# Kernel optimization log

Hardware: AMD Instinct MI355X
Metric: run time of the kernel (lower is better)

## Reference

```python
import jax, jax.numpy as jnp
import numpy as np

B, S, D, H = 4, 2048, 768, 4
DH = D // H  # 192


def setup_inputs() -> dict:
    key = jax.random.key(0)
    ks = jax.random.split(key, 5)
    std = 1.0 / np.sqrt(D)
    return {
        "x": jax.random.normal(ks[0], (B, S, D), dtype=jnp.float32),
        "Wq": jax.random.normal(ks[1], (D, D), dtype=jnp.float32) * std,
        "Wk": jax.random.normal(ks[2], (D, D), dtype=jnp.float32) * std,
        "Wv": jax.random.normal(ks[3], (D, D), dtype=jnp.float32) * std,
        "Wo": jax.random.normal(ks[4], (D, D), dtype=jnp.float32) * std,
    }


def reference(x, Wq, Wk, Wv, Wo):
    b, s, d = x.shape
    # nn.Linear(bias=False): y = x @ W.T
    q = (x @ Wq.T).reshape(b, s, H, DH).transpose(0, 2, 1, 3)  # [B,H,S,DH]
    k = (x @ Wk.T).reshape(b, s, H, DH).transpose(0, 2, 1, 3)
    v = (x @ Wv.T).reshape(b, s, H, DH).transpose(0, 2, 1, 3)
    scale = jnp.sqrt(jnp.asarray(DH, dtype=q.dtype))
    logits = jnp.einsum("bhqd,bhkd->bhqk", q, k) / scale  # [B,H,S,S]
    causal = jnp.tril(jnp.ones((s, s), dtype=bool))
    logits = jnp.where(causal, logits, -jnp.inf)
    A = jax.nn.softmax(logits, axis=-1)
    preout = jnp.einsum("bhqk,bhkd->bhqd", A, v)  # [B,H,S,DH]
    # W_O = rearrange(Wo.T, '(h dh) dm -> h dh dm'); sum over heads == full Wo
    W_O = Wo.T.reshape(H, DH, D)
    out = jnp.einsum("bhsd,hdm->bsm", preout, W_O)  # [B,S,D]
    return out
```

## Files before the change

kernel.cpp:

```cpp
#include <hip/hip_runtime.h>
#include <hip/hip_bf16.h>

constexpr int CB = 4, CS = 2048, CD = 768, CH = 4, CDH = 192;
constexpr int CM = CB * CS;

typedef float f32x4 __attribute__((ext_vector_type(4)));
typedef float fx4 __attribute__((ext_vector_type(4)));
typedef __bf16 bx8 __attribute__((ext_vector_type(8)));
typedef unsigned short u16;
typedef u16 u16x8 __attribute__((ext_vector_type(8)));
typedef u16 u16x4 __attribute__((ext_vector_type(4)));

static __device__ __forceinline__ u16 f32_bf16(float f) {
  unsigned u = __builtin_bit_cast(unsigned, f);
  u += 0x7FFFu + ((u >> 16) & 1u);
  return (u16)(u >> 16);
}
static __device__ __forceinline__ float bf16_f32(u16 v) {
  return __builtin_bit_cast(float, (unsigned)v << 16);
}

static __device__ __forceinline__ f32x4 mfma16(bx8 a, bx8 b, f32x4 c) {
  return __builtin_amdgcn_mfma_f32_16x16x32_bf16(a, b, c, 0, 0, 0);
}

static __device__ __forceinline__ void bar_bare() {
  __builtin_amdgcn_s_barrier();
  __builtin_amdgcn_sched_barrier(0);
}
static __device__ __forceinline__ void bar_lgkm() {
  asm volatile("s_waitcnt lgkmcnt(0)" ::: "memory");
  __builtin_amdgcn_s_barrier();
  __builtin_amdgcn_sched_barrier(0);
}

__global__ void __launch_bounds__(256) convert_all(
    const float* __restrict__ x, const float* __restrict__ wq,
    const float* __restrict__ wk, const float* __restrict__ wv,
    const float* __restrict__ wo, u16* __restrict__ xb, u16* __restrict__ wqb,
    u16* __restrict__ wkb, u16* __restrict__ wvb, u16* __restrict__ wob) {
  const float* srcs[5] = {x, wq, wk, wv, wo};
  u16* dsts[5] = {xb, wqb, wkb, wvb, wob};
  const int n4s[5] = {CM * CD / 4, CD * CD / 4, CD * CD / 4, CD * CD / 4,
                      CD * CD / 4};
  const int gsz = gridDim.x * blockDim.x;
  const int gid = blockIdx.x * blockDim.x + threadIdx.x;
#pragma unroll
  for (int sg = 0; sg < 5; ++sg) {
    const fx4* src = (const fx4*)srcs[sg];
    u16* dst = dsts[sg];
    const int n4 = n4s[sg];
    for (int i = gid; i < n4; i += gsz) {
      fx4 v = src[i];
      u16x4 o;
      o[0] = f32_bf16(v[0]);
      o[1] = f32_bf16(v[1]);
      o[2] = f32_bf16(v[2]);
      o[3] = f32_bf16(v[3]);
      *(u16x4*)&dst[(size_t)i * 4] = o;
    }
  }
}

template <bool OUT_BF16>
__global__ void __launch_bounds__(256) gemm_bt(
    const u16* __restrict__ A, const u16* __restrict__ Bw0,
    const u16* __restrict__ Bw1, const u16* __restrict__ Bw2,
    void* __restrict__ C0, void* __restrict__ C1, void* __restrict__ C2,
    int M, int N, int K) {
  constexpr int LDK = 72;
  __shared__ u16 As[128][LDK];
  __shared__ u16 Bs[128][LDK];
  const int z = blockIdx.z;
  const u16* Bw = (z == 0) ? Bw0 : ((z == 1) ? Bw1 : Bw2);
  void* Cv = (z == 0) ? C0 : ((z == 1) ? C1 : C2);
  const int m0 = blockIdx.x * 128;
  const int n0 = blockIdx.y * 128;
  const int tid = threadIdx.x;
  const int wave = tid >> 6, lane = tid & 63;
  const int wr = wave >> 1, wc = wave & 1;
  const int lr = lane & 15, lhi = lane >> 4;

  f32x4 acc[4][4];
  const f32x4 zero = {0.f, 0.f, 0.f, 0.f};
#pragma unroll
  for (int i = 0; i < 4; ++i)
#pragma unroll
    for (int j = 0; j < 4; ++j) acc[i][j] = zero;

  u16x8 areg[4], breg[4];
  auto ldregs = [&](int kk) {
#pragma unroll
    for (int r = 0; r < 4; ++r) {
      const int id = tid + r * 256;
      const int row = id >> 3, ch = id & 7;
      areg[r] = *(const u16x8*)&A[(size_t)(m0 + row) * K + kk + ch * 8];
      breg[r] = *(const u16x8*)&Bw[(size_t)(n0 + row) * K + kk + ch * 8];
    }
  };

  ldregs(0);
  for (int kk = 0; kk < K; kk += 64) {
    bar_bare();
#pragma unroll
    for (int r = 0; r < 4; ++r) {
      const int id = tid + r * 256;
      const int row = id >> 3, ch = id & 7;
      *(u16x8*)&As[row][ch * 8] = areg[r];
      *(u16x8*)&Bs[row][ch * 8] = breg[r];
    }
    if (kk + 64 < K) ldregs(kk + 64);
    bar_lgkm();
#pragma unroll
    for (int ks = 0; ks < 2; ++ks) {
      bx8 af[4], bf[4];
#pragma unroll
      for (int mf = 0; mf < 4; ++mf)
        af[mf] = *(const bx8*)&As[wr * 64 + mf * 16 + lr][ks * 32 + lhi * 8];
#pragma unroll
      for (int nf = 0; nf < 4; ++nf)
        bf[nf] = *(const bx8*)&Bs[wc * 64 + nf * 16 + lr][ks * 32 + lhi * 8];
      __builtin_amdgcn_s_setprio(1);
#pragma unroll
      for (int mf = 0; mf < 4; ++mf)
#pragma unroll
        for (int nf = 0; nf < 4; ++nf)
          acc[mf][nf] = mfma16(af[mf], bf[nf], acc[mf][nf]);
      __builtin_amdgcn_s_setprio(0);
    }
  }
#pragma unroll
  for (int mf = 0; mf < 4; ++mf)
#pragma unroll
    for (int nf = 0; nf < 4; ++nf)
#pragma unroll
      for (int r = 0; r < 4; ++r) {
        const int row = m0 + wr * 64 + mf * 16 + lhi * 4 + r;
        const int col = n0 + wc * 64 + nf * 16 + lr;
        if constexpr (OUT_BF16)
          ((u16*)Cv)[(size_t)row * N + col] = f32_bf16(acc[mf][nf][r]);
        else
          ((float*)Cv)[(size_t)row * N + col] = acc[mf][nf][r];
      }
}

__global__ void __launch_bounds__(256, 2) flash_attn(
    const u16* __restrict__ Qg, const u16* __restrict__ Kg,
    const u16* __restrict__ Vg, u16* __restrict__ Og, u16* __restrict__ paO,
    float* __restrict__ paML, u16* __restrict__ pbO,
    float* __restrict__ pbML) {
  __shared__ u16 Ks[12288];
  __shared__ u16 Vs[12288];
  const int i0_ = blockIdx.x;
  const int xcd = i0_ & 7;
  const int j_ = i0_ >> 3;
  const int bh = xcd * 2 + (j_ >> 5);
  const int jj = j_ & 31;
  const int t = jj >> 1;
  const int roleB = jj & 1;
  const int qtLo = t, qtHi = 31 - t;
  const int slot = bh * 16 + (15 - t);
  const int b = bh >> 2, h = bh & 3;
  const int tid = threadIdx.x;
  const int wave = tid >> 6, lane = tid & 63;
  const int lr = lane & 15, lhi = lane >> 4;
  const size_t base_elem = ((size_t)b * CS) * CD + (size_t)h * CDH;
  constexpr float scale = 0.07216878364870323f;
  const f32x4 zero = {0.f, 0.f, 0.f, 0.f};

  int kOff[6], vOff[6];
#pragma unroll
  for (int r = 0; r < 6; ++r) {
    const int p = tid + r * 256;
    {
      const int k = p / 24, c16 = p - k * 24;
      const unsigned swz = ((unsigned)(c16 * 16)) ^ ((unsigned)((k & 7) << 4));
      kOff[r] = k * CD + (int)(swz >> 1);
    }
    {
      const int blk = p >> 3, kq = (p >> 1) & 3, dh = p & 1;
      const int kpos = ((blk & 15) << 2) + kq;
      const int kglob = (((kpos >> 5) * 2 + ((kpos >> 2) & 1)) << 4) +
                        (((kpos >> 3) & 3) << 2) + (kpos & 3);
      const int d = ((blk >> 4) << 4) + dh * 8;
      vOff[r] = kglob * CD + d;
    }
  }
  const unsigned vlds0 =
      (unsigned)(unsigned long long)(__attribute__((address_space(3)))
                                         u16*)&Vs[0];

  float m_run, l_run;
  f32x4 acc[12];
  bx8 qf[6];
  u16x8 kreg[6], vreg[6];

  auto qload = [&](int qt) {
    const size_t qoff = base_elem + (size_t)(qt * 64 + wave * 16 + lr) * CD;
#pragma unroll
    for (int c = 0; c < 6; ++c)
      qf[c] = *(const bx8*)&Qg[qoff + c * 32 + lhi * 8];
  };

  auto ldregs = [&](int kt) {
    const u16* kg = Kg + base_elem + (size_t)(kt * 64) * CD;
    const u16* vg = Vg + base_elem + (size_t)(kt * 64) * CD;
#pragma unroll
    for (int r = 0; r < 6; ++r) {
      kreg[r] = *(const u16x8*)&kg[kOff[r]];
      vreg[r] = *(const u16x8*)&vg[vOff[r]];
    }
  };

  auto compute = [&](int i, int qt) {
    const int qg = qt * 64 + wave * 16 + lr;
    const int k0 = i * 64;
    const bool diag = (i == qt);
    f32x4 st[4];
#pragma unroll
    for (int mf = 0; mf < 4; ++mf) st[mf] = zero;
    __builtin_amdgcn_s_setprio(1);
#pragma unroll
    for (int c = 0; c < 6; ++c)
#pragma unroll
      for (int mf = 0; mf < 4; ++mf) {
        const int row = mf * 16 + lr;
        const unsigned off =
            ((unsigned)(c * 64 + lhi * 16)) ^ ((unsigned)((row & 7) << 4));
        const bx8 kf =
            *(const bx8*)((const char*)Ks + (size_t)row * 384 + off);
        st[mf] = mfma16(kf, qf[c], st[mf]);
      }
    __builtin_amdgcn_s_setprio(0);
    float pvv[16];
#pragma unroll
    for (int mf = 0; mf < 4; ++mf)
#pragma unroll
      for (int r = 0; r < 4; ++r) {
        float s = st[mf][r] * scale;
        if (diag && (k0 + mf * 16 + lhi * 4 + r > qg)) s = -INFINITY;
        pvv[mf * 4 + r] = s;
      }
    float mx = pvv[0];
#pragma unroll
    for (int tt = 1; tt < 16; ++tt) mx = fmaxf(mx, pvv[tt]);
    mx = fmaxf(mx, __shfl_xor(mx, 16, 64));
    mx = fmaxf(mx, __shfl_xor(mx, 32, 64));
    const bool skip = __all(mx - m_run <= 8.0f);
    if (!skip) {
      const float mnew = fmaxf(m_run, mx);
      const float alpha = __expf(m_run - mnew);
      float afr[4];
#pragma unroll
      for (int r = 0; r < 4; ++r) afr[r] = __shfl(alpha, lhi * 4 + r, 64);
#pragma unroll
      for (int nf = 0; nf < 12; ++nf)
#pragma unroll
        for (int r = 0; r < 4; ++r) acc[nf][r] *= afr[r];
      l_run *= alpha;
      m_run = mnew;
    }
    float rs = 0.f;
#pragma unroll
    for (int tt = 0; tt < 16; ++tt) {
      const float e = __expf(pvv[tt] - m_run);
      pvv[tt] = e;
      rs += e;
    }
    rs += __shfl_xor(rs, 16, 64);
    rs += __shfl_xor(rs, 32, 64);
    l_run += rs;
    u16x8 pa0, pa1;
#pragma unroll
    for (int j = 0; j < 8; ++j) {
      pa0[j] = f32_bf16(pvv[j]);
      pa1[j] = f32_bf16(pvv[8 + j]);
    }
    const bx8 pf0 = __builtin_bit_cast(bx8, pa0);
    const bx8 pf1 = __builtin_bit_cast(bx8, pa1);
#pragma unroll
    for (int gg = 0; gg < 3; ++gg) {
      u16x4 tl[4][2], th[4][2];
#pragma unroll
      for (int q4 = 0; q4 < 4; ++q4)
#pragma unroll
        for (int c2 = 0; c2 < 2; ++c2) {
          const int nf = gg * 4 + q4;
          const unsigned va =
              vlds0 + (unsigned)((nf * 16 + c2 * 8 + lhi * 2) * 128 + lr * 8);
          asm volatile("ds_read_b64_tr_b16 %0, %2\n\t"
                       "ds_read_b64_tr_b16 %1, %2 offset:128"
                       : "=&v"(tl[q4][c2]), "=&v"(th[q4][c2])
                       : "v"(va));
        }
      asm volatile("s_waitcnt lgkmcnt(0)" ::: "memory");
      __builtin_amdgcn_sched_barrier(0);
      __builtin_amdgcn_s_setprio(1);
#pragma unroll
      for (int q4 = 0; q4 < 4; ++q4)
#pragma unroll
        for (int c2 = 0; c2 < 2; ++c2) {
          const int nf = gg * 4 + q4;
          const u16x8 vv = __builtin_shufflevector(tl[q4][c2], th[q4][c2], 0,
                                                   1, 2, 3, 4, 5, 6, 7);
          acc[nf] = mfma16(c2 == 0 ? pf0 : pf1, __builtin_bit_cast(bx8, vv),
                           acc[nf]);
        }
      __builtin_amdgcn_s_setprio(0);
    }
  };

  auto run = [&](int qt, int i0, int i1) {
    m_run = -INFINITY;
    l_run = 0.f;
#pragma unroll
    for (int nf = 0; nf < 12; ++nf) acc[nf] = zero;
    qload(qt);
    ldregs(i0);
    for (int i = i0; i <= i1; ++i) {
      bar_bare();
#pragma unroll
      for (int r = 0; r < 6; ++r) {
        *(u16x8*)&Ks[(size_t)(tid + r * 256) * 8] = kreg[r];
        *(u16x8*)&Vs[(size_t)(tid + r * 256) * 8] = vreg[r];
      }
      if (i < i1) ldregs(i + 1);
      bar_lgkm();
      compute(i, qt);
    }
  };

  auto final_epilogue = [&](int qt) {
#pragma unroll
    for (int r = 0; r < 4; ++r) {
      const float lb = __shfl(l_run, lhi * 4 + r, 64);
      const float linv = 1.0f / lb;
      const size_t orow =
          base_elem + (size_t)(qt * 64 + wave * 16 + lhi * 4 + r) * CD;
#pragma unroll
      for (int nf = 0; nf < 12; ++nf)
        Og[orow + nf * 16 + lr] = f32_bf16(acc[nf][r] * linv);
    }
  };

  auto partial_epilogue = [&](u16* pO, float* pML) {
    if (lhi == 0) {
      pML[slot * 128 + wave * 16 + lr] = m_run;
      pML[slot * 128 + 64 + wave * 16 + lr] = l_run;
    }
#pragma unroll
    for (int r = 0; r < 4; ++r) {
      const float lb = __shfl(l_run, lhi * 4 + r, 64);
      const float linv = 1.0f / lb;
      u16* dst =
          pO + (size_t)slot * 12288 + (size_t)(wave * 16 + lhi * 4 + r) * 192;
#pragma unroll
      for (int nf = 0; nf < 12; ++nf)
        dst[nf * 16 + lr] = f32_bf16(acc[nf][r] * linv);
    }
  };

  if (roleB) {
    run(qtHi, 15 - t, 31 - t);
    partial_epilogue(pbO, pbML);
  } else {
    run(qtLo, 0, t);
    final_epilogue(qtLo);
    if (t < 15) {
      run(qtHi, 0, 14 - t);
      partial_epilogue(paO, paML);
    } else {
      if (tid < 64) {
        paML[slot * 128 + tid] = -1e30f;
        paML[slot * 128 + 64 + tid] = 0.f;
      }
    }
  }
}

__global__ void __launch_bounds__(256) combine_qt(
    const u16* __restrict__ paO, const float* __restrict__ paML,
    const u16* __restrict__ pbO, const float* __restrict__ pbML,
    u16* __restrict__ Og) {
  const int s = blockIdx.x;
  const int bh = s >> 4;
  const int qtHi = 16 + (s & 15);
  const int b = bh >> 2, h = bh & 3;
  const int tid = threadIdx.x;
  const int row = tid >> 2, cg = tid & 3;
  const float mA = paML[s * 128 + row], lA = paML[s * 128 + 64 + row];
  const float mB = pbML[s * 128 + row], lB = pbML[s * 128 + 64 + row];
  const size_t obase =
      ((size_t)b * CS + (size_t)qtHi * 64 + row) * CD + h * CDH + cg * 48;
  const u16* pa = paO + (size_t)s * 12288 + (size_t)row * 192 + cg * 48;
  const u16* pb = pbO + (size_t)s * 12288 + (size_t)row * 192 + cg * 48;
  if (lA > 0.f) {
    const float M = fmaxf(mA, mB);
    const float wA = lA * __expf(mA - M), wB = lB * __expf(mB - M);
    const float inv = 1.0f / (wA + wB);
    const float fa = wA * inv, fb = wB * inv;
#pragma unroll
    for (int c = 0; c < 6; ++c) {
      const u16x8 va = *(const u16x8*)&pa[c * 8];
      const u16x8 vb = *(const u16x8*)&pb[c * 8];
      u16x8 o;
#pragma unroll
      for (int j = 0; j < 8; ++j)
        o[j] = f32_bf16(fa * bf16_f32(va[j]) + fb * bf16_f32(vb[j]));
      *(u16x8*)&Og[obase + c * 8] = o;
    }
  } else {
#pragma unroll
    for (int c = 0; c < 6; ++c)
      *(u16x8*)&Og[obase + c * 8] = *(const u16x8*)&pb[c * 8];
  }
}

extern "C" void kernel_launch(void* const* d_in, const int* in_sizes, int n_in,
                              void* d_out, int out_size, void* d_ws,
                              size_t ws_size, hipStream_t stream) {
  (void)in_sizes;
  (void)n_in;
  (void)out_size;
  (void)ws_size;
  const float* x = (const float*)d_in[0];
  const float* wq = (const float*)d_in[1];
  const float* wk = (const float*)d_in[2];
  const float* wv = (const float*)d_in[3];
  const float* wo = (const float*)d_in[4];
  float* out = (float*)d_out;
  char* ws = (char*)d_ws;
  const size_t big = (size_t)CM * CD * 2;
  const size_t wsz = (size_t)CD * CD * 2;
  u16* xb = (u16*)ws;
  u16* qb = (u16*)(ws + big);
  u16* kb = (u16*)(ws + 2 * big);
  u16* vb = (u16*)(ws + 3 * big);
  u16* wqb = (u16*)(ws + 4 * big);
  u16* wkb = (u16*)(ws + 4 * big + wsz);
  u16* wvb = (u16*)(ws + 4 * big + 2 * wsz);
  u16* wob = (u16*)(ws + 4 * big + 3 * wsz);
  u16* pob = xb;
  const size_t pOsz = (size_t)256 * 64 * 192 * 2;
  u16* paO = (u16*)d_out;
  u16* pbO = (u16*)((char*)d_out + pOsz);
  float* paML = (float*)((char*)d_out + 2 * pOsz);
  float* pbML = (float*)((char*)d_out + 2 * pOsz + 131072);

  convert_all<<<dim3(2048), dim3(256), 0, stream>>>(x, wq, wk, wv, wo, xb, wqb,
                                                    wkb, wvb, wob);
  gemm_bt<true><<<dim3(64, 6, 3), dim3(256), 0, stream>>>(
      xb, wqb, wkb, wvb, (void*)qb, (void*)kb, (void*)vb, CM, CD, CD);
  flash_attn<<<dim3(512), dim3(256), 0, stream>>>(qb, kb, vb, pob, paO, paML,
                                                  pbO, pbML);
  combine_qt<<<dim3(256), dim3(256), 0, stream>>>(paO, paML, pbO, pbML, pob);
  gemm_bt<false><<<dim3(64, 6, 1), dim3(256), 0, stream>>>(
      pob, wob, wob, wob, (void*)out, (void*)out, (void*)out, CM, CD, CD);
}
```

Before: 132.7 us.

## Stage K/V tiles with direct global-to-LDS loads into double-buffered shared memory

After: 162.3 us. 1.22x slower.

```diff
diff --git a/kernel.cpp b/kernel.cpp
--- a/kernel.cpp
+++ b/kernel.cpp
@@ -24,12 +24,23 @@
   return __builtin_amdgcn_mfma_f32_16x16x32_bf16(a, b, c, 0, 0, 0);
 }
 
+static __device__ __forceinline__ void load_lds16(const u16* g, u16* l) {
+  __builtin_amdgcn_global_load_lds(
+      (const __attribute__((address_space(1))) unsigned int*)g,
+      (__attribute__((address_space(3))) unsigned int*)l, 16, 0, 0);
+}
+
 static __device__ __forceinline__ void bar_bare() {
   __builtin_amdgcn_s_barrier();
   __builtin_amdgcn_sched_barrier(0);
 }
 static __device__ __forceinline__ void bar_lgkm() {
   asm volatile("s_waitcnt lgkmcnt(0)" ::: "memory");
+  __builtin_amdgcn_s_barrier();
+  __builtin_amdgcn_sched_barrier(0);
+}
+static __device__ __forceinline__ void bar_vm0() {
+  asm volatile("s_waitcnt vmcnt(0)" ::: "memory");
   __builtin_amdgcn_s_barrier();
   __builtin_amdgcn_sched_barrier(0);
 }
@@ -149,8 +160,8 @@
     const u16* __restrict__ Vg, u16* __restrict__ Og, u16* __restrict__ paO,
     float* __restrict__ paML, u16* __restrict__ pbO,
     float* __restrict__ pbML) {
-  __shared__ u16 Ks[12288];
-  __shared__ u16 Vs[12288];
+  __shared__ u16 Ks[2][12288];
+  __shared__ u16 Vs[2][12288];
   const int i0_ = blockIdx.x;
   const int xcd = i0_ & 7;
   const int j_ = i0_ >> 3;
@@ -188,12 +199,11 @@
   }
   const unsigned vlds0 =
       (unsigned)(unsigned long long)(__attribute__((address_space(3)))
-                                         u16*)&Vs[0];
+                                         u16*)&Vs[0][0];
 
   float m_run, l_run;
   f32x4 acc[12];
   bx8 qf[6];
-  u16x8 kreg[6], vreg[6];
 
   auto qload = [&](int qt) {
     const size_t qoff = base_elem + (size_t)(qt * 64 + wave * 16 + lr) * CD;
@@ -202,20 +212,22 @@
       qf[c] = *(const bx8*)&Qg[qoff + c * 32 + lhi * 8];
   };
 
-  auto ldregs = [&](int kt) {
+  auto stage = [&](int buf, int kt) {
     const u16* kg = Kg + base_elem + (size_t)(kt * 64) * CD;
     const u16* vg = Vg + base_elem + (size_t)(kt * 64) * CD;
 #pragma unroll
-    for (int r = 0; r < 6; ++r) {
-      kreg[r] = *(const u16x8*)&kg[kOff[r]];
-      vreg[r] = *(const u16x8*)&vg[vOff[r]];
-    }
-  };
-
-  auto compute = [&](int i, int qt) {
+    for (int r = 0; r < 6; ++r)
+      load_lds16(kg + kOff[r], &Ks[buf][(size_t)(tid + r * 256) * 8]);
+#pragma unroll
+    for (int r = 0; r < 6; ++r)
+      load_lds16(vg + vOff[r], &Vs[buf][(size_t)(tid + r * 256) * 8]);
+  };
+
+  auto compute = [&](int i, int qt, int cur) {
     const int qg = qt * 64 + wave * 16 + lr;
     const int k0 = i * 64;
     const bool diag = (i == qt);
+    const char* ksb = (const char*)&Ks[cur][0];
     f32x4 st[4];
 #pragma unroll
     for (int mf = 0; mf < 4; ++mf) st[mf] = zero;
@@ -227,8 +239,7 @@
         const int row = mf * 16 + lr;
         const unsigned off =
             ((unsigned)(c * 64 + lhi * 16)) ^ ((unsigned)((row & 7) << 4));
-        const bx8 kf =
-            *(const bx8*)((const char*)Ks + (size_t)row * 384 + off);
+        const bx8 kf = *(const bx8*)(ksb + (size_t)row * 384 + off);
         st[mf] = mfma16(kf, qf[c], st[mf]);
       }
     __builtin_amdgcn_s_setprio(0);
@@ -278,6 +289,7 @@
     }
     const bx8 pf0 = __builtin_bit_cast(bx8, pa0);
     const bx8 pf1 = __builtin_bit_cast(bx8, pa1);
+    const unsigned vbb = vlds0 + (unsigned)cur * 24576u;
 #pragma unroll
     for (int gg = 0; gg < 3; ++gg) {
       u16x4 tl[4][2], th[4][2];
@@ -287,7 +299,7 @@
         for (int c2 = 0; c2 < 2; ++c2) {
           const int nf = gg * 4 + q4;
           const unsigned va =
-              vlds0 + (unsigned)((nf * 16 + c2 * 8 + lhi * 2) * 128 + lr * 8);
+              vbb + (unsigned)((nf * 16 + c2 * 8 + lhi * 2) * 128 + lr * 8);
           asm volatile("ds_read_b64_tr_b16 %0, %2\n\t"
                        "ds_read_b64_tr_b16 %1, %2 offset:128"
                        : "=&v"(tl[q4][c2]), "=&v"(th[q4][c2])
@@ -316,17 +328,13 @@
 #pragma unroll
     for (int nf = 0; nf < 12; ++nf) acc[nf] = zero;
     qload(qt);
-    ldregs(i0);
+    bar_bare();
+    stage(0, i0);
     for (int i = i0; i <= i1; ++i) {
-      bar_bare();
-#pragma unroll
-      for (int r = 0; r < 6; ++r) {
-        *(u16x8*)&Ks[(size_t)(tid + r * 256) * 8] = kreg[r];
-        *(u16x8*)&Vs[(size_t)(tid + r * 256) * 8] = vreg[r];
-      }
-      if (i < i1) ldregs(i + 1);
-      bar_lgkm();
-      compute(i, qt);
+      const int cur = (i - i0) & 1;
+      bar_vm0();
+      if (i < i1) stage(cur ^ 1, i + 1);
+      compute(i, qt, cur);
     }
   };
 
```

## Rebalance causal flash attention into split-KV work items with heaviest first

Applied to the files above, without the earlier changes.

Result: slower. 135.9 us (+2.4%).

```diff
diff --git a/kernel.cpp b/kernel.cpp
--- a/kernel.cpp
+++ b/kernel.cpp
@@ -146,20 +146,30 @@
 
 __global__ void __launch_bounds__(256, 2) flash_attn(
     const u16* __restrict__ Qg, const u16* __restrict__ Kg,
-    const u16* __restrict__ Vg, u16* __restrict__ Og, u16* __restrict__ paO,
-    float* __restrict__ paML, u16* __restrict__ pbO,
-    float* __restrict__ pbML) {
+    const u16* __restrict__ Vg, u16* __restrict__ Og, u16* __restrict__ pO,
+    float* __restrict__ pML) {
   __shared__ u16 Ks[12288];
   __shared__ u16 Vs[12288];
   const int i0_ = blockIdx.x;
   const int xcd = i0_ & 7;
-  const int j_ = i0_ >> 3;
-  const int bh = xcd * 2 + (j_ >> 5);
-  const int jj = j_ & 31;
-  const int t = jj >> 1;
-  const int roleB = jj & 1;
-  const int qtLo = t, qtHi = 31 - t;
-  const int slot = bh * 16 + (15 - t);
+  const int r_ = i0_ >> 3;
+  const int bh = xcd * 2 + (r_ & 1);
+  const int s = 55 - (r_ >> 1);
+  int qt, k0, k1, pidx;
+  if (s < 8) {
+    qt = s;
+    k0 = 0;
+    k1 = qt + 1;
+    pidx = -1;
+  } else {
+    const int u = s - 8;
+    qt = 8 + (u >> 1);
+    const int half = u & 1;
+    const int L = qt + 1, h0 = L >> 1;
+    k0 = half ? h0 : 0;
+    k1 = half ? L : h0;
+    pidx = u;
+  }
   const int b = bh >> 2, h = bh & 3;
   const int tid = threadIdx.x;
   const int wave = tid >> 6, lane = tid & 63;
@@ -190,17 +200,19 @@
       (unsigned)(unsigned long long)(__attribute__((address_space(3)))
                                          u16*)&Vs[0];
 
-  float m_run, l_run;
+  float m_run = -INFINITY, l_run = 0.f;
   f32x4 acc[12];
+#pragma unroll
+  for (int nf = 0; nf < 12; ++nf) acc[nf] = zero;
   bx8 qf[6];
   u16x8 kreg[6], vreg[6];
 
-  auto qload = [&](int qt) {
+  {
     const size_t qoff = base_elem + (size_t)(qt * 64 + wave * 16 + lr) * CD;
 #pragma unroll
     for (int c = 0; c < 6; ++c)
       qf[c] = *(const bx8*)&Qg[qoff + c * 32 + lhi * 8];
-  };
+  }
 
   auto ldregs = [&](int kt) {
     const u16* kg = Kg + base_elem + (size_t)(kt * 64) * CD;
@@ -212,9 +224,19 @@
     }
   };
 
-  auto compute = [&](int i, int qt) {
-    const int qg = qt * 64 + wave * 16 + lr;
-    const int k0 = i * 64;
+  const int qg = qt * 64 + wave * 16 + lr;
+  ldregs(k0);
+  for (int i = k0; i < k1; ++i) {
+    bar_bare();
+#pragma unroll
+    for (int r = 0; r < 6; ++r) {
+      *(u16x8*)&Ks[(size_t)(tid + r * 256) * 8] = kreg[r];
+      *(u16x8*)&Vs[(size_t)(tid + r * 256) * 8] = vreg[r];
+    }
+    if (i + 1 < k1) ldregs(i + 1);
+    bar_lgkm();
+
+    const int kb0 = i * 64;
     const bool diag = (i == qt);
     f32x4 st[4];
 #pragma unroll
@@ -237,9 +259,9 @@
     for (int mf = 0; mf < 4; ++mf)
 #pragma unroll
       for (int r = 0; r < 4; ++r) {
-        float s = st[mf][r] * scale;
-        if (diag && (k0 + mf * 16 + lhi * 4 + r > qg)) s = -INFINITY;
-        pvv[mf * 4 + r] = s;
+        float sv = st[mf][r] * scale;
+        if (diag && (kb0 + mf * 16 + lhi * 4 + r > qg)) sv = -INFINITY;
+        pvv[mf * 4 + r] = sv;
       }
     float mx = pvv[0];
 #pragma unroll
@@ -308,29 +330,9 @@
         }
       __builtin_amdgcn_s_setprio(0);
     }
-  };
-
-  auto run = [&](int qt, int i0, int i1) {
-    m_run = -INFINITY;
-    l_run = 0.f;
-#pragma unroll
-    for (int nf = 0; nf < 12; ++nf) acc[nf] = zero;
-    qload(qt);
-    ldregs(i0);
-    for (int i = i0; i <= i1; ++i) {
-      bar_bare();
-#pragma unroll
-      for (int r = 0; r < 6; ++r) {
-        *(u16x8*)&Ks[(size_t)(tid + r * 256) * 8] = kreg[r];
-        *(u16x8*)&Vs[(size_t)(tid + r * 256) * 8] = vreg[r];
-      }
-      if (i < i1) ldregs(i + 1);
-      bar_lgkm();
-      compute(i, qt);
-    }
-  };
-
-  auto final_epilogue = [&](int qt) {
+  }
+
+  if (pidx < 0) {
 #pragma unroll
     for (int r = 0; r < 4; ++r) {
       const float lb = __shfl(l_run, lhi * 4 + r, 64);
@@ -341,9 +343,8 @@
       for (int nf = 0; nf < 12; ++nf)
         Og[orow + nf * 16 + lr] = f32_bf16(acc[nf][r] * linv);
     }
-  };
-
-  auto partial_epilogue = [&](u16* pO, float* pML) {
+  } else {
+    const int slot = bh * 48 + pidx;
     if (lhi == 0) {
       pML[slot * 128 + wave * 16 + lr] = m_run;
       pML[slot * 128 + 64 + wave * 16 + lr] = l_run;
@@ -358,61 +359,41 @@
       for (int nf = 0; nf < 12; ++nf)
         dst[nf * 16 + lr] = f32_bf16(acc[nf][r] * linv);
     }
-  };
-
-  if (roleB) {
-    run(qtHi, 15 - t, 31 - t);
-    partial_epilogue(pbO, pbML);
-  } else {
-    run(qtLo, 0, t);
-    final_epilogue(qtLo);
-    if (t < 15) {
-      run(qtHi, 0, 14 - t);
-      partial_epilogue(paO, paML);
-    } else {
-      if (tid < 64) {
-        paML[slot * 128 + tid] = -1e30f;
-        paML[slot * 128 + 64 + tid] = 0.f;
-      }
-    }
   }
 }
 
 __global__ void __launch_bounds__(256) combine_qt(
-    const u16* __restrict__ paO, const float* __restrict__ paML,
-    const u16* __restrict__ pbO, const float* __restrict__ pbML,
+    const u16* __restrict__ pO, const float* __restrict__ pML,
     u16* __restrict__ Og) {
-  const int s = blockIdx.x;
-  const int bh = s >> 4;
-  const int qtHi = 16 + (s & 15);
+  const int c = blockIdx.x;
+  const int xcd = c & 7;
+  const int t2 = c >> 3;
+  const int bh = xcd * 2 + (t2 & 1);
+  const int qt = 8 + (t2 >> 1);
   const int b = bh >> 2, h = bh & 3;
+  const int u0 = (qt - 8) * 2;
+  const int p0 = bh * 48 + u0, p1 = p0 + 1;
   const int tid = threadIdx.x;
   const int row = tid >> 2, cg = tid & 3;
-  const float mA = paML[s * 128 + row], lA = paML[s * 128 + 64 + row];
-  const float mB = pbML[s * 128 + row], lB = pbML[s * 128 + 64 + row];
+  const float mA = pML[p0 * 128 + row], lA = pML[p0 * 128 + 64 + row];
+  const float mB = pML[p1 * 128 + row], lB = pML[p1 * 128 + 64 + row];
+  const float M = fmaxf(mA, mB);
+  const float wA = lA * __expf(mA - M), wB = lB * __expf(mB - M);
+  const float inv = 1.0f / (wA + wB);
+  const float fa = wA * inv, fb = wB * inv;
   const size_t obase =
-      ((size_t)b * CS + (size_t)qtHi * 64 + row) * CD + h * CDH + cg * 48;
-  const u16* pa = paO + (size_t)s * 12288 + (size_t)row * 192 + cg * 48;
-  const u16* pb = pbO + (size_t)s * 12288 + (size_t)row * 192 + cg * 48;
-  if (lA > 0.f) {
-    const float M = fmaxf(mA, mB);
-    const float wA = lA * __expf(mA - M), wB = lB * __expf(mB - M);
-    const float inv = 1.0f / (wA + wB);
-    const float fa = wA * inv, fb = wB * inv;
-#pragma unroll
-    for (int c = 0; c < 6; ++c) {
-      const u16x8 va = *(const u16x8*)&pa[c * 8];
-      const u16x8 vb = *(const u16x8*)&pb[c * 8];
-      u16x8 o;
-#pragma unroll
-      for (int j = 0; j < 8; ++j)
-        o[j] = f32_bf16(fa * bf16_f32(va[j]) + fb * bf16_f32(vb[j]));
-      *(u16x8*)&Og[obase + c * 8] = o;
-    }
-  } else {
-#pragma unroll
-    for (int c = 0; c < 6; ++c)
-      *(u16x8*)&Og[obase + c * 8] = *(const u16x8*)&pb[c * 8];
+      ((size_t)b * CS + (size_t)qt * 64 + row) * CD + h * CDH + cg * 48;
+  const u16* pa = pO + (size_t)p0 * 12288 + (size_t)row * 192 + cg * 48;
+  const u16* pb = pO + (size_t)p1 * 12288 + (size_t)row * 192 + cg * 48;
+#pragma unroll
+  for (int cc = 0; cc < 6; ++cc) {
+    const u16x8 va = *(const u16x8*)&pa[cc * 8];
+    const u16x8 vb = *(const u16x8*)&pb[cc * 8];
+    u16x8 o;
+#pragma unroll
+    for (int j = 0; j < 8; ++j)
+      o[j] = f32_bf16(fa * bf16_f32(va[j]) + fb * bf16_f32(vb[j]));
+    *(u16x8*)&Og[obase + cc * 8] = o;
   }
 }
 
@@ -441,19 +422,15 @@
   u16* wvb = (u16*)(ws + 4 * big + 2 * wsz);
   u16* wob = (u16*)(ws + 4 * big + 3 * wsz);
   u16* pob = xb;
-  const size_t pOsz = (size_t)256 * 64 * 192 * 2;
-  u16* paO = (u16*)d_out;
-  u16* pbO = (u16*)((char*)d_out + pOsz);
-  float* paML = (float*)((char*)d_out + 2 * pOsz);
-  float* pbML = (float*)((char*)d_out + 2 * pOsz + 131072);
+  u16* pO = (u16*)d_out;
+  float* pML = (float*)((char*)d_out + (size_t)768 * 24576);
 
   convert_all<<<dim3(2048), dim3(256), 0, stream>>>(x, wq, wk, wv, wo, xb, wqb,
                                                     wkb, wvb, wob);
   gemm_bt<true><<<dim3(64, 6, 3), dim3(256), 0, stream>>>(
       xb, wqb, wkb, wvb, (void*)qb, (void*)kb, (void*)vb, CM, CD, CD);
-  flash_attn<<<dim3(512), dim3(256), 0, stream>>>(qb, kb, vb, pob, paO, paML,
-                                                  pbO, pbML);
-  combine_qt<<<dim3(256), dim3(256), 0, stream>>>(paO, paML, pbO, pbML, pob);
+  flash_attn<<<dim3(896), dim3(256), 0, stream>>>(qb, kb, vb, pob, pO, pML);
+  combine_qt<<<dim3(384), dim3(256), 0, stream>>>(pO, pML, pob);
   gemm_bt<false><<<dim3(64, 6, 1), dim3(256), 0, stream>>>(
       pob, wob, wob, wob, (void*)out, (void*)out, (void*)out, CM, CD, CD);
 }
```

## Double-buffer K tiles in LDS and defer V barrier until PV stage

Applied to the files above, without the earlier changes.

Measured after the change: 137.9 us. 3.9% more time.

```diff
diff --git a/kernel.cpp b/kernel.cpp
--- a/kernel.cpp
+++ b/kernel.cpp
@@ -149,7 +149,7 @@
     const u16* __restrict__ Vg, u16* __restrict__ Og, u16* __restrict__ paO,
     float* __restrict__ paML, u16* __restrict__ pbO,
     float* __restrict__ pbML) {
-  __shared__ u16 Ks[12288];
+  __shared__ u16 Kb[2][12288];
   __shared__ u16 Vs[12288];
   const int i0_ = blockIdx.x;
   const int xcd = i0_ & 7;
@@ -202,20 +202,22 @@
       qf[c] = *(const bx8*)&Qg[qoff + c * 32 + lhi * 8];
   };
 
-  auto ldregs = [&](int kt) {
+  auto kload = [&](int kt) {
     const u16* kg = Kg + base_elem + (size_t)(kt * 64) * CD;
+#pragma unroll
+    for (int r = 0; r < 6; ++r) kreg[r] = *(const u16x8*)&kg[kOff[r]];
+  };
+  auto vload = [&](int kt) {
     const u16* vg = Vg + base_elem + (size_t)(kt * 64) * CD;
 #pragma unroll
-    for (int r = 0; r < 6; ++r) {
-      kreg[r] = *(const u16x8*)&kg[kOff[r]];
-      vreg[r] = *(const u16x8*)&vg[vOff[r]];
-    }
-  };
-
-  auto compute = [&](int i, int qt) {
+    for (int r = 0; r < 6; ++r) vreg[r] = *(const u16x8*)&vg[vOff[r]];
+  };
+
+  auto compute = [&](int i, int qt, int cur) {
     const int qg = qt * 64 + wave * 16 + lr;
     const int k0 = i * 64;
     const bool diag = (i == qt);
+    const char* ksb = (const char*)&Kb[cur][0];
     f32x4 st[4];
 #pragma unroll
     for (int mf = 0; mf < 4; ++mf) st[mf] = zero;
@@ -227,8 +229,7 @@
         const int row = mf * 16 + lr;
         const unsigned off =
             ((unsigned)(c * 64 + lhi * 16)) ^ ((unsigned)((row & 7) << 4));
-        const bx8 kf =
-            *(const bx8*)((const char*)Ks + (size_t)row * 384 + off);
+        const bx8 kf = *(const bx8*)(ksb + (size_t)row * 384 + off);
         st[mf] = mfma16(kf, qf[c], st[mf]);
       }
     __builtin_amdgcn_s_setprio(0);
@@ -278,6 +279,7 @@
     }
     const bx8 pf0 = __builtin_bit_cast(bx8, pa0);
     const bx8 pf1 = __builtin_bit_cast(bx8, pa1);
+    bar_lgkm();
 #pragma unroll
     for (int gg = 0; gg < 3; ++gg) {
       u16x4 tl[4][2], th[4][2];
@@ -316,17 +318,28 @@
 #pragma unroll
     for (int nf = 0; nf < 12; ++nf) acc[nf] = zero;
     qload(qt);
-    ldregs(i0);
+    kload(i0);
+    bar_bare();
+#pragma unroll
+    for (int r = 0; r < 6; ++r)
+      *(u16x8*)&Kb[0][(size_t)(tid + r * 256) * 8] = kreg[r];
+    vload(i0);
+    if (i0 < i1) kload(i0 + 1);
+    bar_lgkm();
     for (int i = i0; i <= i1; ++i) {
+      const int cur = (i - i0) & 1;
       bar_bare();
 #pragma unroll
-      for (int r = 0; r < 6; ++r) {
-        *(u16x8*)&Ks[(size_t)(tid + r * 256) * 8] = kreg[r];
+      for (int r = 0; r < 6; ++r)
         *(u16x8*)&Vs[(size_t)(tid + r * 256) * 8] = vreg[r];
+      if (i < i1) {
+#pragma unroll
+        for (int r = 0; r < 6; ++r)
+          *(u16x8*)&Kb[cur ^ 1][(size_t)(tid + r * 256) * 8] = kreg[r];
+        vload(i + 1);
       }
-      if (i < i1) ldregs(i + 1);
-      bar_lgkm();
-      compute(i, qt);
+      if (i + 1 < i1) kload(i + 2);
+      compute(i, qt, cur);
     }
   };
 
```
